# Kernel tuning notes

Measured on AMD Instinct MI355X. Metric: run time of the kernel, lower is better.

Reference implementation:

```python
import jax, jax.numpy as jnp
import numpy as np

B, N, D, H = 8, 1024, 512, 8
DH = D // H


def setup_inputs() -> dict:
    key = jax.random.key(0)
    ks = jax.random.split(key, 7)
    s = 1.0 / np.sqrt(D)
    return {
        "x": jax.random.normal(ks[0], (B, N, D), dtype=jnp.float32),
        "Wq": jax.random.normal(ks[1], (D, D), dtype=jnp.float32) * s,
        "bq": jax.random.normal(ks[2], (D,), dtype=jnp.float32) * 0.01,
        "Wk": jax.random.normal(ks[3], (D, D), dtype=jnp.float32) * s,
        "bk": jax.random.normal(ks[4], (D,), dtype=jnp.float32) * 0.01,
        "Wv": jax.random.normal(ks[5], (D, D), dtype=jnp.float32) * s,
        "bv": jax.random.normal(ks[6], (D,), dtype=jnp.float32) * 0.01,
    }


def reference(x, Wq, bq, Wk, bk, Wv, bv):
    # Q/K/V projections (nn.Linear: x @ W^T + b; here W stored as [in, out])
    q = x @ Wq + bq  # [B, N, D]
    k = x @ Wk + bk
    v = x @ Wv + bv
    # chunk(dim=2)+cat(dim=0) == split channels into H head groups
    q = q.reshape(B, N, H, DH)
    k = k.reshape(B, N, H, DH)
    v = v.reshape(B, N, H, DH)
    # NOTE: original applies NO 1/sqrt(head_dim) scaling
    scores = jnp.einsum("bqhd,bkhd->bhqk", q, k)  # [B, H, N, N]
    weights = jax.nn.softmax(scores, axis=-1)
    y = jnp.einsum("bhqk,bkhd->bqhd", weights, v)  # [B, N, H, DH]
    return y.reshape(B, N, D)
```

## Files before the change

### kernel.cpp

```cpp
#include <hip/hip_runtime.h>
#include <hip/hip_bf16.h>

typedef _Float16 half8 __attribute__((ext_vector_type(8)));
typedef _Float16 half4v __attribute__((ext_vector_type(4)));
typedef float floatx4 __attribute__((ext_vector_type(4)));

#define BB 8
#define NN 1024
#define DD 512
#define HH 8
#define DHH 64

__device__ __forceinline__ void gload_lds16(const _Float16* g, _Float16* l) {
    __builtin_amdgcn_global_load_lds(
        (const __attribute__((address_space(1))) void*)g,
        (__attribute__((address_space(3))) void*)l, 16, 0, 0);
}

__global__ __launch_bounds__(256) void cvt_kernel(const float* __restrict__ x,
                                                  const float* __restrict__ Wq,
                                                  const float* __restrict__ Wk,
                                                  const float* __restrict__ Wv,
                                                  _Float16* __restrict__ xh,
                                                  _Float16* __restrict__ Wt) {
    __shared__ __align__(16) _Float16 tb[64][72];
    int bx = blockIdx.x;
    int tid = threadIdx.x;
    if (bx < 4096) {
        int i = bx * 256 + tid;
        float4 v = ((const float4*)x)[i];
        half4v o;
        o[0] = (_Float16)v.x; o[1] = (_Float16)v.y;
        o[2] = (_Float16)v.z; o[3] = (_Float16)v.w;
        ((half4v*)xh)[i] = o;
        return;
    }
    int t = bx - 4096;
    int which = t >> 6;
    int rem = t & 63;
    int kt = (rem >> 3) * 64, nt = (rem & 7) * 64;
    const float* W = (which == 0) ? Wq : (which == 1) ? Wk : Wv;
    _Float16* Wto = Wt + (size_t)which * DD * DD;
    for (int i = 0; i < 16; i++) {
        int idx = tid + i * 256;
        int r = idx >> 6, c = idx & 63;
        tb[c][r] = (_Float16)W[(size_t)(kt + r) * DD + nt + c];
    }
    __syncthreads();
    for (int i = 0; i < 16; i++) {
        int idx = tid + i * 256;
        int r = idx >> 6, c = idx & 63;
        Wto[(size_t)(nt + r) * DD + kt + c] = tb[r][c];
    }
}

__global__ __launch_bounds__(256) void qkv_gemm_kernel(const _Float16* __restrict__ xh,
                                                       const _Float16* __restrict__ Wt,
                                                       const float* __restrict__ bq,
                                                       const float* __restrict__ bk,
                                                       const float* __restrict__ bv,
                                                       _Float16* __restrict__ QKV) {
    __shared__ __align__(16) _Float16 As[128 * 32];
    __shared__ __align__(16) _Float16 Bs[128 * 32];

    int which = blockIdx.z;
    const _Float16* Wtw = Wt + (size_t)which * DD * DD;
    const float* bias = (which == 0) ? bq : (which == 1) ? bk : bv;

    int tid = threadIdx.x;
    int wave = tid >> 6, lane = tid & 63;
    int quad = lane >> 4, l16 = lane & 15;
    int wm = wave >> 1, wn = wave & 1;
    int mBase = blockIdx.y * 128;
    int nBase = blockIdx.x * 128;

    int srow = wave * 32 + (lane >> 2);
    int scol = (lane & 3) * 8;
    const _Float16* ag = (which < 2)
        ? Wtw + (size_t)(nBase + srow) * DD + scol
        : xh  + (size_t)(mBase + srow) * DD + scol;
    const _Float16* bg = (which < 2)
        ? xh  + (size_t)(mBase + srow) * DD + scol
        : Wtw + (size_t)(nBase + srow) * DD + scol;
    _Float16* al = As + (wave * 32) * 32;
    _Float16* bl = Bs + (wave * 32) * 32;

    floatx4 acc[4][4];
    for (int i = 0; i < 4; i++)
        for (int j = 0; j < 4; j++) acc[i][j] = (floatx4){0.f, 0.f, 0.f, 0.f};

    for (int kk = 0; kk < DD; kk += 32) {
        __syncthreads();
        gload_lds16(ag + kk,            al);
        gload_lds16(ag + 16 * DD + kk,  al + 16 * 32);
        gload_lds16(bg + kk,            bl);
        gload_lds16(bg + 16 * DD + kk,  bl + 16 * 32);
        __syncthreads();

        half8 af[4], bf[4];
        for (int i = 0; i < 4; i++)
            af[i] = *(const half8*)&As[(wm * 64 + i * 16 + l16) * 32 + quad * 8];
        for (int j = 0; j < 4; j++)
            bf[j] = *(const half8*)&Bs[(wn * 64 + j * 16 + l16) * 32 + quad * 8];
        for (int i = 0; i < 4; i++)
            for (int j = 0; j < 4; j++)
                acc[i][j] = __builtin_amdgcn_mfma_f32_16x16x32_f16(af[i], bf[j], acc[i][j], 0, 0, 0);
    }

    if (which < 2) {
        _Float16* out = QKV + (size_t)which * (BB * NN) * DD;
        for (int i = 0; i < 4; i++) {
            int feat0 = nBase + wm * 64 + i * 16 + quad * 4;
            float4 b4 = *(const float4*)&bias[feat0];
            for (int j = 0; j < 4; j++) {
                int token = mBase + wn * 64 + j * 16 + l16;
                half4v pack;
                pack[0] = (_Float16)(acc[i][j][0] + b4.x);
                pack[1] = (_Float16)(acc[i][j][1] + b4.y);
                pack[2] = (_Float16)(acc[i][j][2] + b4.z);
                pack[3] = (_Float16)(acc[i][j][3] + b4.w);
                *(half4v*)&out[(size_t)token * DD + feat0] = pack;
            }
        }
    } else {
        _Float16* VT = QKV + (size_t)2 * (BB * NN) * DD;
        for (int j = 0; j < 4; j++) {
            int col = nBase + wn * 64 + j * 16 + l16;
            float bval = bias[col];
            for (int i = 0; i < 4; i++) {
                int row0 = mBase + wm * 64 + i * 16 + quad * 4;
                int b = row0 >> 10;
                int n = row0 & 1023;
                half4v pack;
                for (int reg = 0; reg < 4; reg++) pack[reg] = (_Float16)(acc[i][j][reg] + bval);
                *(half4v*)&VT[((size_t)b * 512 + col) * 1024 + n] = pack;
            }
        }
    }
}

__global__ __launch_bounds__(256) void attn_kernel(const _Float16* __restrict__ QKV,
                                                   float* __restrict__ out) {
    const _Float16* Q  = QKV;
    const _Float16* K  = QKV + (size_t)(BB * NN) * DD;
    const _Float16* VT = QKV + (size_t)2 * (BB * NN) * DD;

    __shared__ __align__(16) _Float16 Kt[128 * 64];
    __shared__ __align__(16) _Float16 Vt[64 * 128];
    __shared__ __align__(16) _Float16 PT[4][16 * 64];

    int tid = threadIdx.x;
    int wave = tid >> 6, lane = tid & 63;
    int quad = lane >> 4, l16 = lane & 15;
    int qt = blockIdx.x, h = blockIdx.y, b = blockIdx.z;

    const _Float16* Qb  = Q + ((size_t)b * NN) * DD + h * DHH;
    const _Float16* Kb  = K + ((size_t)b * NN) * DD + h * DHH;
    const _Float16* VTb = VT + ((size_t)b * 512 + h * 64) * 1024;

    int qrow = qt * 64 + wave * 16 + l16;
    half8 qf0 = *(const half8*)(Qb + (size_t)qrow * DD + 0 * 32 + quad * 8);
    half8 qf1 = *(const half8*)(Qb + (size_t)qrow * DD + 1 * 32 + quad * 8);

    floatx4 o[4];
    for (int nt = 0; nt < 4; nt++) o[nt] = (floatx4){0.f, 0.f, 0.f, 0.f};
    float m_i = -1e30f, l_i = 0.f;

    const _Float16* kg = Kb + (size_t)(wave * 32 + (lane >> 3)) * DD
                            + ((lane & 7) ^ (lane >> 3)) * 8;
    _Float16* kl = Kt + (wave * 32) * 64;
    _Float16* vl = Vt + (wave * 16) * 128;
    int l16sw = l16 & 7;

    for (int kt = 0; kt < 8; kt++) {
        __syncthreads();
        for (int i = 0; i < 4; i++)
            gload_lds16(kg + (size_t)(kt * 128 + i * 8) * DD, kl + (i * 8) * 64);
        for (int i = 0; i < 4; i++) {
            int vrow = wave * 16 + i * 4 + (lane >> 4);
            int vc = (lane & 15) ^ (i * 4 + (lane >> 4));
            gload_lds16(VTb + (size_t)vrow * 1024 + kt * 128 + vc * 8, vl + (i * 4) * 128);
        }
        __syncthreads();

        floatx4 s[8];
        for (int nt = 0; nt < 8; nt++) s[nt] = (floatx4){0.f, 0.f, 0.f, 0.f};
        for (int ks = 0; ks < 2; ks++) {
            half8 qf = ks ? qf1 : qf0;
            for (int nt = 0; nt < 8; nt++) {
                half8 kf = *(const half8*)&Kt[(nt * 16 + l16) * 64
                                              + (((ks * 4 + quad) ^ l16sw) * 8)];
                s[nt] = __builtin_amdgcn_mfma_f32_16x16x32_f16(kf, qf, s[nt], 0, 0, 0);
            }
        }

        float mx = -1e30f;
        for (int nt = 0; nt < 8; nt++)
            for (int r = 0; r < 4; r++) mx = fmaxf(mx, s[nt][r]);
        mx = fmaxf(mx, __shfl_xor(mx, 16, 64));
        mx = fmaxf(mx, __shfl_xor(mx, 32, 64));
        float mnew = fmaxf(m_i, mx);
        float alpha = __expf(m_i - mnew);
        m_i = mnew;
        float rs = 0.f;
        for (int nt = 0; nt < 8; nt++)
            for (int r = 0; r < 4; r++) {
                float p = __expf(s[nt][r] - mnew);
                s[nt][r] = p;
                rs += p;
            }
        rs += __shfl_xor(rs, 16, 64);
        rs += __shfl_xor(rs, 32, 64);
        l_i = l_i * alpha + rs;

        for (int nt = 0; nt < 4; nt++)
            for (int r = 0; r < 4; r++) o[nt][r] *= alpha;

        for (int hh = 0; hh < 2; hh++) {
            for (int ntl = 0; ntl < 4; ntl++) {
                floatx4 sv = s[hh * 4 + ntl];
                half4v p4;
                for (int r = 0; r < 4; r++) p4[r] = (_Float16)sv[r];
                *(half4v*)&PT[wave][l16 * 64 + (((2 * ntl + (quad >> 1)) ^ l16sw) * 8)
                               + (quad & 1) * 4] = p4;
            }
            for (int ks2h = 0; ks2h < 2; ks2h++) {
                half8 pf = *(const half8*)&PT[wave][l16 * 64
                                                   + (((ks2h * 4 + quad) ^ l16sw) * 8)];
                int ks2 = hh * 2 + ks2h;
                for (int nt = 0; nt < 4; nt++) {
                    half8 vf = *(const half8*)&Vt[(nt * 16 + l16) * 128
                                                  + (((ks2 * 4 + quad) ^ l16) * 8)];
                    o[nt] = __builtin_amdgcn_mfma_f32_16x16x32_f16(vf, pf, o[nt], 0, 0, 0);
                }
            }
        }
    }

    float inv = 1.0f / l_i;
    float* outb = out + ((size_t)b * NN) * DD + h * DHH;
    int row = qt * 64 + wave * 16 + l16;
    for (int nt = 0; nt < 4; nt++) {
        float4 st;
        st.x = o[nt][0] * inv; st.y = o[nt][1] * inv;
        st.z = o[nt][2] * inv; st.w = o[nt][3] * inv;
        *(float4*)&outb[(size_t)row * DD + nt * 16 + quad * 4] = st;
    }
}

extern "C" void kernel_launch(void* const* d_in, const int* in_sizes, int n_in,
                              void* d_out, int out_size, void* d_ws, size_t ws_size,
                              hipStream_t stream) {
    const float* x  = (const float*)d_in[0];
    const float* Wq = (const float*)d_in[1];
    const float* bq = (const float*)d_in[2];
    const float* Wk = (const float*)d_in[3];
    const float* bk = (const float*)d_in[4];
    const float* Wv = (const float*)d_in[5];
    const float* bv = (const float*)d_in[6];
    float* out = (float*)d_out;

    _Float16* xh  = (_Float16*)d_ws;
    _Float16* Wt  = xh + (size_t)(BB * NN) * DD;
    _Float16* QKV = Wt + (size_t)3 * DD * DD;

    hipLaunchKernelGGL(cvt_kernel, dim3(4096 + 192), dim3(256), 0, stream,
                       x, Wq, Wk, Wv, xh, Wt);
    hipLaunchKernelGGL(qkv_gemm_kernel, dim3(4, 64, 3), dim3(256), 0, stream,
                       xh, Wt, bq, bk, bv, QKV);
    hipLaunchKernelGGL(attn_kernel, dim3(16, 8, 8), dim3(256), 0, stream, QKV, out);
}
```

Baseline: 140.9 us.

## Double-buffer K/V tiles in attention with smaller 64-key tiles

The attention loop now uses two LDS buffers of 64-key K and V^T tiles instead of one 128-key tile. The next tile is prefetched with global_load_lds right after the single per-iteration barrier, so the load overlaps the current tile's QK^T, softmax and PV MFMAs. This also halves the barriers per iteration. In exchange it runs twice as many iterations with more online-softmax rescale overhead, and the barrier still drains all outstanding loads.

```diff
diff --git a/kernel.cpp b/kernel.cpp
--- a/kernel.cpp
+++ b/kernel.cpp
@@ -139,19 +139,30 @@
     }
 }
 
+__device__ __forceinline__ void stage_kv(const _Float16* kg, const _Float16* vg,
+                                         _Float16* kl, _Float16* vl, int kt) {
+    const _Float16* kgk = kg + (size_t)(kt * 64) * DD;
+    const _Float16* vgk = vg + kt * 64;
+    gload_lds16(kgk,            kl);
+    gload_lds16(kgk + 8 * DD,   kl + 8 * 64);
+    gload_lds16(vgk,            vl);
+    gload_lds16(vgk + 8 * 1024, vl + 8 * 64);
+}
+
 __global__ __launch_bounds__(256) void attn_kernel(const _Float16* __restrict__ QKV,
                                                    float* __restrict__ out) {
     const _Float16* Q  = QKV;
     const _Float16* K  = QKV + (size_t)(BB * NN) * DD;
     const _Float16* VT = QKV + (size_t)2 * (BB * NN) * DD;
 
-    __shared__ __align__(16) _Float16 Kt[128 * 64];
-    __shared__ __align__(16) _Float16 Vt[64 * 128];
+    __shared__ __align__(16) _Float16 Kt[2][64 * 64];
+    __shared__ __align__(16) _Float16 Vt[2][64 * 64];
     __shared__ __align__(16) _Float16 PT[4][16 * 64];
 
     int tid = threadIdx.x;
     int wave = tid >> 6, lane = tid & 63;
     int quad = lane >> 4, l16 = lane & 15;
+    int l16sw = l16 & 7;
     int qt = blockIdx.x, h = blockIdx.y, b = blockIdx.z;
 
     const _Float16* Qb  = Q + ((size_t)b * NN) * DD + h * DHH;
@@ -166,44 +177,45 @@
     for (int nt = 0; nt < 4; nt++) o[nt] = (floatx4){0.f, 0.f, 0.f, 0.f};
     float m_i = -1e30f, l_i = 0.f;
 
-    const _Float16* kg = Kb + (size_t)(wave * 32 + (lane >> 3)) * DD
-                            + ((lane & 7) ^ (lane >> 3)) * 8;
-    _Float16* kl = Kt + (wave * 32) * 64;
-    _Float16* vl = Vt + (wave * 16) * 128;
-    int l16sw = l16 & 7;
-
-    for (int kt = 0; kt < 8; kt++) {
+    int srow = lane >> 3;
+    int schunk = (lane & 7) ^ srow;
+    const _Float16* kg = Kb + (size_t)(wave * 16 + srow) * DD + schunk * 8;
+    const _Float16* vg = VTb + (size_t)(wave * 16 + srow) * 1024 + schunk * 8;
+    _Float16* kl0 = &Kt[0][(wave * 16) * 64];
+    _Float16* vl0 = &Vt[0][(wave * 16) * 64];
+    _Float16* kl1 = &Kt[1][(wave * 16) * 64];
+    _Float16* vl1 = &Vt[1][(wave * 16) * 64];
+
+    stage_kv(kg, vg, kl0, vl0, 0);
+
+    for (int kt = 0; kt < 16; kt++) {
+        int cur = kt & 1;
         __syncthreads();
-        for (int i = 0; i < 4; i++)
-            gload_lds16(kg + (size_t)(kt * 128 + i * 8) * DD, kl + (i * 8) * 64);
-        for (int i = 0; i < 4; i++) {
-            int vrow = wave * 16 + i * 4 + (lane >> 4);
-            int vc = (lane & 15) ^ (i * 4 + (lane >> 4));
-            gload_lds16(VTb + (size_t)vrow * 1024 + kt * 128 + vc * 8, vl + (i * 4) * 128);
-        }
-        __syncthreads();
-
-        floatx4 s[8];
-        for (int nt = 0; nt < 8; nt++) s[nt] = (floatx4){0.f, 0.f, 0.f, 0.f};
+        if (kt + 1 < 16)
+            stage_kv(kg, vg, cur ? kl0 : kl1, cur ? vl0 : vl1, kt + 1);
+
+        floatx4 s[4];
+        for (int nt = 0; nt < 4; nt++) s[nt] = (floatx4){0.f, 0.f, 0.f, 0.f};
         for (int ks = 0; ks < 2; ks++) {
             half8 qf = ks ? qf1 : qf0;
-            for (int nt = 0; nt < 8; nt++) {
-                half8 kf = *(const half8*)&Kt[(nt * 16 + l16) * 64
-                                              + (((ks * 4 + quad) ^ l16sw) * 8)];
+            for (int nt = 0; nt < 4; nt++) {
+                half8 kf = *(const half8*)&Kt[cur][(nt * 16 + l16) * 64
+                                                   + (((ks * 4 + quad) ^ l16sw) * 8)];
                 s[nt] = __builtin_amdgcn_mfma_f32_16x16x32_f16(kf, qf, s[nt], 0, 0, 0);
             }
         }
 
         float mx = -1e30f;
-        for (int nt = 0; nt < 8; nt++)
+        for (int nt = 0; nt < 4; nt++)
             for (int r = 0; r < 4; r++) mx = fmaxf(mx, s[nt][r]);
         mx = fmaxf(mx, __shfl_xor(mx, 16, 64));
         mx = fmaxf(mx, __shfl_xor(mx, 32, 64));
         float mnew = fmaxf(m_i, mx);
         float alpha = __expf(m_i - mnew);
         m_i = mnew;
+
         float rs = 0.f;
-        for (int nt = 0; nt < 8; nt++)
+        for (int nt = 0; nt < 4; nt++)
             for (int r = 0; r < 4; r++) {
                 float p = __expf(s[nt][r] - mnew);
                 s[nt][r] = p;
@@ -216,23 +228,19 @@
         for (int nt = 0; nt < 4; nt++)
             for (int r = 0; r < 4; r++) o[nt][r] *= alpha;
 
-        for (int hh = 0; hh < 2; hh++) {
-            for (int ntl = 0; ntl < 4; ntl++) {
-                floatx4 sv = s[hh * 4 + ntl];
-                half4v p4;
-                for (int r = 0; r < 4; r++) p4[r] = (_Float16)sv[r];
-                *(half4v*)&PT[wave][l16 * 64 + (((2 * ntl + (quad >> 1)) ^ l16sw) * 8)
+        for (int ntl = 0; ntl < 4; ntl++) {
+            half4v p4;
+            for (int r = 0; r < 4; r++) p4[r] = (_Float16)s[ntl][r];
+            *(half4v*)&PT[wave][l16 * 64 + (((ntl * 2 + (quad >> 1)) ^ l16sw) * 8)
                                + (quad & 1) * 4] = p4;
-            }
-            for (int ks2h = 0; ks2h < 2; ks2h++) {
-                half8 pf = *(const half8*)&PT[wave][l16 * 64
-                                                   + (((ks2h * 4 + quad) ^ l16sw) * 8)];
-                int ks2 = hh * 2 + ks2h;
-                for (int nt = 0; nt < 4; nt++) {
-                    half8 vf = *(const half8*)&Vt[(nt * 16 + l16) * 128
-                                                  + (((ks2 * 4 + quad) ^ l16) * 8)];
-                    o[nt] = __builtin_amdgcn_mfma_f32_16x16x32_f16(vf, pf, o[nt], 0, 0, 0);
-                }
+        }
+
+        for (int ks2 = 0; ks2 < 2; ks2++) {
+            half8 pf = *(const half8*)&PT[wave][l16 * 64 + (((ks2 * 4 + quad) ^ l16sw) * 8)];
+            for (int nt = 0; nt < 4; nt++) {
+                half8 vf = *(const half8*)&Vt[cur][(nt * 16 + l16) * 64
+                                                   + (((ks2 * 4 + quad) ^ l16sw) * 8)];
+                o[nt] = __builtin_amdgcn_mfma_f32_16x16x32_f16(vf, pf, o[nt], 0, 0, 0);
             }
         }
     }
```

After: 141.8 us. No clear change (+0.6%).
